# Kernel optimization log

Hardware: AMD Instinct MI355X
Metric: run time of the kernel (lower is better)

Reference implementation:

```python
import jax, jax.numpy as jnp
import numpy as np

N_EMBD = 1024
N_HEAD = 16
HEAD_DIM = N_EMBD // N_HEAD  # 64
N_CTX = 2048
ROPE_THETA = 10000.0


def _rope_cache(L, dim, base):
    inv_freq = 1.0 / (base ** (np.arange(0, dim, 2, dtype=np.float32) / dim))
    t = np.arange(L, dtype=np.float32)
    freqs = np.einsum('i,j->ij', t, inv_freq)  # (L, dim/2)
    return jnp.asarray(np.cos(freqs)), jnp.asarray(np.sin(freqs))


def _apply_rotary(x, cos, sin):
    # x: (B, H, L, D), cos/sin: (L, D/2) -> broadcast (1,1,L,D/2)
    x1 = x[..., ::2]
    x2 = x[..., 1::2]
    c = cos[None, None, :, :]
    s = sin[None, None, :, :]
    y1 = x1 * c - x2 * s
    y2 = x1 * s + x2 * c
    # interleave back: stack on last dim then flatten
    return jnp.stack((y1, y2), axis=-1).reshape(x.shape)


def setup_inputs() -> dict:
    key = jax.random.key(0)
    k1, k2, k3, k4, k5 = jax.random.split(key, 5)
    B, L, D = 4, 2048, N_EMBD
    scale = 0.02
    x = jax.random.normal(k1, (B, L, D), dtype=jnp.float32)
    W_qkv = jax.random.normal(k2, (D, 3 * D), dtype=jnp.float32) * scale
    b_qkv = jnp.zeros((3 * D,), dtype=jnp.float32)
    W_proj = jax.random.normal(k3, (D, D), dtype=jnp.float32) * scale
    b_proj = jnp.zeros((D,), dtype=jnp.float32)
    attention_mask = jnp.ones((B, L), dtype=jnp.int32)
    return {"x": x, "W_qkv": W_qkv, "b_qkv": b_qkv, "W_proj": W_proj,
            "b_proj": b_proj, "attention_mask": attention_mask}


def reference(x, W_qkv, b_qkv, W_proj, b_proj, attention_mask):
    B, L, D = x.shape
    H, Dh = N_HEAD, HEAD_DIM
    qkv = x @ W_qkv + b_qkv  # (B, L, 3D)
    q, k, v = jnp.split(qkv, 3, axis=2)
    # (B, L, H, Dh) -> (B, H, L, Dh)
    q = q.reshape(B, L, H, Dh).transpose(0, 2, 1, 3)
    k = k.reshape(B, L, H, Dh).transpose(0, 2, 1, 3)
    v = v.reshape(B, L, H, Dh).transpose(0, 2, 1, 3)
    cos, sin = _rope_cache(L, Dh, ROPE_THETA)
    q = _apply_rotary(q, cos, sin)
    k = _apply_rotary(k, cos, sin)
    # mask: causal & key padding keep
    causal = jnp.tril(jnp.ones((L, L), dtype=bool))[None, None]        # (1,1,L,L)
    key_keep = attention_mask.astype(bool)[:, None, None, :]          # (B,1,1,L)
    keep = causal & key_keep                                          # (B,1,L,L)
    scores = jnp.einsum('bhqd,bhkd->bhqk', q, k) / jnp.sqrt(jnp.float32(Dh))
    scores = jnp.where(keep, scores, jnp.finfo(scores.dtype).min)
    attn = jax.nn.softmax(scores, axis=-1)
    out = jnp.einsum('bhqk,bhkd->bhqd', attn, v)  # (B,H,L,Dh)
    out = out.transpose(0, 2, 1, 3).reshape(B, L, D)
    return out @ W_proj + b_proj
```

## Files before the change

kernel.cpp:

```cpp
#include <hip/hip_runtime.h>
#include <math.h>

typedef __bf16 bf16x8 __attribute__((ext_vector_type(8)));
typedef float f32x4 __attribute__((ext_vector_type(4)));
typedef float f32x16 __attribute__((ext_vector_type(16)));
typedef unsigned short u16;
typedef unsigned short u16x8 __attribute__((ext_vector_type(8)));
typedef unsigned short u16x4 __attribute__((ext_vector_type(4)));
typedef unsigned u32x2v __attribute__((ext_vector_type(2)));

#define BATCH 4
#define SEQ   2048
#define EMBD  1024
#define NHEAD 16
#define HDIM  64
#define MROWS 8192
#define QKVN  3072

__device__ __forceinline__ u16 f2bf(float f) {
    union { float f; unsigned u; } cv; cv.f = f;
    unsigned u = cv.u;
    return (u16)((u + 0x7FFFu + ((u >> 16) & 1u)) >> 16);
}

__device__ __forceinline__ unsigned cvtpk_bf16(float lo, float hi) {
    unsigned r;
    asm("v_cvt_pk_bf16_f32 %0, %1, %2" : "=v"(r) : "v"(lo), "v"(hi));
    return r;
}

__device__ __forceinline__ void glds16(const void* g, void* l) {
    __builtin_amdgcn_global_load_lds(
        (const __attribute__((address_space(1))) unsigned int*)(g),
        (__attribute__((address_space(3))) unsigned int*)(l), 16, 0, 0);
}

#define MF8(qm, A0, A1, A2, A3, B0, B1)                                          \
    acc[(qm)*4+0][0] = __builtin_amdgcn_mfma_f32_16x16x32_bf16(A0, B0, acc[(qm)*4+0][0], 0, 0, 0); \
    acc[(qm)*4+0][1] = __builtin_amdgcn_mfma_f32_16x16x32_bf16(A0, B1, acc[(qm)*4+0][1], 0, 0, 0); \
    acc[(qm)*4+1][0] = __builtin_amdgcn_mfma_f32_16x16x32_bf16(A1, B0, acc[(qm)*4+1][0], 0, 0, 0); \
    acc[(qm)*4+1][1] = __builtin_amdgcn_mfma_f32_16x16x32_bf16(A1, B1, acc[(qm)*4+1][1], 0, 0, 0); \
    acc[(qm)*4+2][0] = __builtin_amdgcn_mfma_f32_16x16x32_bf16(A2, B0, acc[(qm)*4+2][0], 0, 0, 0); \
    acc[(qm)*4+2][1] = __builtin_amdgcn_mfma_f32_16x16x32_bf16(A2, B1, acc[(qm)*4+2][1], 0, 0, 0); \
    acc[(qm)*4+3][0] = __builtin_amdgcn_mfma_f32_16x16x32_bf16(A3, B0, acc[(qm)*4+3][0], 0, 0, 0); \
    acc[(qm)*4+3][1] = __builtin_amdgcn_mfma_f32_16x16x32_bf16(A3, B1, acc[(qm)*4+3][1], 0, 0, 0);

__device__ __forceinline__ void transpose_body(const float* __restrict__ W,
                                               u16* __restrict__ Wt, int K, int N,
                                               int n0, int k0, u16 (*T)[68]) {
    const int tx = threadIdx.x & 15, ty = threadIdx.x >> 4;
#pragma unroll
    for (int r = 0; r < 4; r++) {
        int k = k0 + ty + r * 16;
        float4 w = *(const float4*)&W[(size_t)k * N + n0 + tx * 4];
        T[tx * 4 + 0][ty + r * 16] = f2bf(w.x);
        T[tx * 4 + 1][ty + r * 16] = f2bf(w.y);
        T[tx * 4 + 2][ty + r * 16] = f2bf(w.z);
        T[tx * 4 + 3][ty + r * 16] = f2bf(w.w);
    }
    __syncthreads();
#pragma unroll
    for (int r = 0; r < 4; r++) {
        int nl = ty + r * 16;
        u16x4 v = { T[nl][tx * 4 + 0], T[nl][tx * 4 + 1],
                    T[nl][tx * 4 + 2], T[nl][tx * 4 + 3] };
        *(u16x4*)&Wt[(size_t)(n0 + nl) * K + k0 + tx * 4] = v;
    }
}

__global__ __launch_bounds__(256)
void prep_kernel(const float* __restrict__ x, const float* __restrict__ Wqkv,
                 const float* __restrict__ Wproj, const int* __restrict__ amask,
                 u16* __restrict__ Xb, u16* __restrict__ Wqkvt, u16* __restrict__ Wprojt,
                 float* __restrict__ ropeC, float* __restrict__ ropeS,
                 float* __restrict__ mbias, int* __restrict__ flags) {
    __shared__ union { u16 T[64][68]; int ok[4]; } sm;
    const int bx = blockIdx.x, tid = threadIdx.x;
    if (bx < 8192) {
        int i = bx * 256 + tid;
        float4 v = ((const float4*)x)[i];
        u16x4 o = { f2bf(v.x), f2bf(v.y), f2bf(v.z), f2bf(v.w) };
        ((u16x4*)Xb)[i] = o;
    } else if (bx < 8960) {
        int bxx = bx - 8192;
        transpose_body(Wqkv, Wqkvt, EMBD, QKVN, (bxx % 48) * 64, (bxx / 48) * 64, sm.T);
    } else if (bx < 9216) {
        int bxx = bx - 8960;
        transpose_body(Wproj, Wprojt, EMBD, EMBD, (bxx & 15) * 64, (bxx >> 4) * 64, sm.T);
    } else if (bx < 9472) {
        int i = (bx - 9216) * 256 + tid;
        int l = i >> 5, p = i & 31;
        float invf = powf(10000.0f, -(float)(2 * p) * (1.0f / 64.0f));
        float sv, cv;
        sincosf((float)l * invf, &sv, &cv);
        ropeC[i] = cv; ropeS[i] = sv;
    } else {
        int idx = (bx - 9472) * 256 + tid;
        int mv = amask[idx];
        mbias[idx] = mv ? 0.0f : -1e30f;
        unsigned long long bal = __ballot(mv != 0);
        int wv = tid >> 6;
        if ((tid & 63) == 0) sm.ok[wv] = (bal == 0xFFFFFFFFFFFFFFFFull);
        __syncthreads();
        if (tid == 0)   flags[idx >> 7] = sm.ok[0] & sm.ok[1];
        if (tid == 128) flags[idx >> 7] = sm.ok[2] & sm.ok[3];
    }
}

__global__ __launch_bounds__(512, 2)
void qkv_gemm(const u16* __restrict__ A, const u16* __restrict__ Bt,
              const float* __restrict__ bias,
              const float* __restrict__ Ct, const float* __restrict__ St,
              u16* __restrict__ Qo, u16* __restrict__ Ko, u16* __restrict__ Vo) {
    __shared__ u16 SM[49152];
    const int tid = threadIdx.x;
    const int w = tid >> 6, ln = tid & 63;
    const int quad = ln >> 4, l16 = ln & 15;
    const int wm = w >> 2, wn = w & 3;
    const int bid = blockIdx.y * 24 + blockIdx.x;
    const int swz = (bid & 7) * 96 + (bid >> 3);
    const int m0 = (swz / 24) * 256, n0 = (swz % 24) * 128;

    const int sr8 = ln >> 3;
    const int xs = (ln & 7) ^ sr8;
    const u16* Ab = A  + (size_t)(m0 + w * 8 + sr8) * EMBD + xs * 8;
    const u16* Bb = Bt + (size_t)(n0 + w * 8 + sr8) * EMBD + xs * 8;
    u16* ldsA = SM + w * 512;
    u16* ldsB = SM + 32768 + w * 512;
    const int ch0 = ((0 + quad) ^ (l16 & 7)) * 8;
    const int ch1 = ((4 + quad) ^ (l16 & 7)) * 8;

    auto stageA = [&](int buf, int rb, int kt) {
        glds16(Ab + (size_t)rb * EMBD + kt * 64, ldsA + buf * 16384 + rb * 64);
    };
    auto stageB = [&](int buf, int rb, int kt) {
        glds16(Bb + (size_t)rb * EMBD + kt * 64, ldsB + buf * 8192 + rb * 64);
    };

    f32x4 acc[8][2] = {};

    stageA(0, 0, 0);  stageA(0, 128, 0);
    stageA(0, 64, 0); stageA(0, 192, 0);
    stageB(0, 0, 0);  stageB(0, 64, 0);
    stageA(1, 0, 1);  stageA(1, 128, 1);
    asm volatile("s_waitcnt vmcnt(2)" ::: "memory");
    __builtin_amdgcn_sched_barrier(0);
    __builtin_amdgcn_s_barrier();

    for (int u = 0; u < 16; ++u) {
        const int c = u & 1, nc = c ^ 1;
        const u16* Ac0 = SM + c * 16384 + (wm * 128 + l16) * 64;
        const u16* Ac1 = Ac0 + 64 * 64;
        const u16* Bc  = SM + 32768 + c * 8192 + (wn * 32 + l16) * 64;
        bf16x8 a0, a1, a2, a3, bk0a, bk0b, bk1a, bk1b;
        a0 = *(const bf16x8*)&Ac0[ch0];        a1 = *(const bf16x8*)&Ac0[1024 + ch0];
        a2 = *(const bf16x8*)&Ac0[2048 + ch0]; a3 = *(const bf16x8*)&Ac0[3072 + ch0];
        bk0a = *(const bf16x8*)&Bc[ch0];       bk0b = *(const bf16x8*)&Bc[1024 + ch0];
        if (u < 15) { stageA(nc, 64, u + 1); stageA(nc, 192, u + 1); stageB(nc, 64, u + 1); }
        __builtin_amdgcn_sched_barrier(0);
        __builtin_amdgcn_s_setprio(1);
        MF8(0, a0, a1, a2, a3, bk0a, bk0b);
        __builtin_amdgcn_s_setprio(0);
        __builtin_amdgcn_sched_barrier(0);
        a0 = *(const bf16x8*)&Ac0[ch1];        a1 = *(const bf16x8*)&Ac0[1024 + ch1];
        a2 = *(const bf16x8*)&Ac0[2048 + ch1]; a3 = *(const bf16x8*)&Ac0[3072 + ch1];
        bk1a = *(const bf16x8*)&Bc[ch1];       bk1b = *(const bf16x8*)&Bc[1024 + ch1];
        if (u < 15) stageB(nc, 0, u + 1);
        __builtin_amdgcn_sched_barrier(0);
        __builtin_amdgcn_s_setprio(1);
        MF8(0, a0, a1, a2, a3, bk1a, bk1b);
        __builtin_amdgcn_s_setprio(0);
        __builtin_amdgcn_sched_barrier(0);
        __builtin_amdgcn_s_barrier();
        a0 = *(const bf16x8*)&Ac1[ch0];        a1 = *(const bf16x8*)&Ac1[1024 + ch0];
        a2 = *(const bf16x8*)&Ac1[2048 + ch0]; a3 = *(const bf16x8*)&Ac1[3072 + ch0];
        if (u < 14) { stageA(c, 0, u + 2); stageA(c, 128, u + 2); }
        __builtin_amdgcn_sched_barrier(0);
        __builtin_amdgcn_s_setprio(1);
        MF8(1, a0, a1, a2, a3, bk0a, bk0b);
        __builtin_amdgcn_s_setprio(0);
        __builtin_amdgcn_sched_barrier(0);
        a0 = *(const bf16x8*)&Ac1[ch1];        a1 = *(const bf16x8*)&Ac1[1024 + ch1];
        a2 = *(const bf16x8*)&Ac1[2048 + ch1]; a3 = *(const bf16x8*)&Ac1[3072 + ch1];
        __builtin_amdgcn_sched_barrier(0);
        __builtin_amdgcn_s_setprio(1);
        MF8(1, a0, a1, a2, a3, bk1a, bk1b);
        __builtin_amdgcn_s_setprio(0);
        __builtin_amdgcn_sched_barrier(0);
        if (u < 14) asm volatile("s_waitcnt vmcnt(2)" ::: "memory");
        else        asm volatile("s_waitcnt vmcnt(0)" ::: "memory");
        __builtin_amdgcn_sched_barrier(0);
        __builtin_amdgcn_s_barrier();
    }

    const int sec = n0 >> 10;
    if (sec == 2) {
#pragma unroll
        for (int ii = 0; ii < 8; ii++)
#pragma unroll
            for (int r = 0; r < 4; r++) {
                int m = m0 + wm * 128 + ii * 16 + quad * 4 + r;
                int b = m >> 11, l = m & 2047;
#pragma unroll
                for (int j = 0; j < 2; j++) {
                    int n = n0 + wn * 32 + j * 16 + l16;
                    int dcol = n & 1023;
                    int h = dcol >> 6, dh = dcol & 63;
                    float v = acc[ii][j][r] + bias[n];
                    Vo[(((size_t)b * NHEAD + h) * SEQ + l) * HDIM + dh] = f2bf(v);
                }
            }
    } else {
        u16* O = (sec == 0) ? Qo : Ko;
        const float qs = (sec == 0) ? 0.125f * 1.44269504f : 1.0f;
#pragma unroll
        for (int ii = 0; ii < 8; ii++)
#pragma unroll
            for (int r = 0; r < 4; r++) {
                int m = m0 + wm * 128 + ii * 16 + quad * 4 + r;
                int b = m >> 11, l = m & 2047;
#pragma unroll
                for (int j = 0; j < 2; j++) {
                    int n = n0 + wn * 32 + j * 16 + l16;
                    int h = (n & 1023) >> 6, dh = n & 63;
                    int p = (n & 63) >> 1;
                    float v = acc[ii][j][r] + bias[n];
                    float pv = __shfl_xor(v, 1, 64);
                    float cv = Ct[l * 32 + p], sv = St[l * 32 + p];
                    float o = (l16 & 1) ? (pv * sv + v * cv) : (v * cv - pv * sv);
                    O[(((size_t)b * NHEAD + h) * SEQ + l) * HDIM + dh] = f2bf(o * qs);
                }
            }
    }
}

__global__ __launch_bounds__(256)
void transpose_v(const u16* __restrict__ Vo, u16* __restrict__ Vt) {
    __shared__ u16 T[64][72];
    const int bh = blockIdx.y;
    const int l0 = blockIdx.x * 64;
    const int tx = threadIdx.x & 15, ty = threadIdx.x >> 4;
#pragma unroll
    for (int rr = 0; rr < 4; rr++) {
        int l = ty + rr * 16;
        u16x4 v = *(const u16x4*)&Vo[((size_t)bh * SEQ + l0 + l) * HDIM + tx * 4];
        T[l][tx * 4 + 0] = v.x; T[l][tx * 4 + 1] = v.y;
        T[l][tx * 4 + 2] = v.z; T[l][tx * 4 + 3] = v.w;
    }
    __syncthreads();
#pragma unroll
    for (int rr = 0; rr < 4; rr++) {
        int dh = ty + rr * 16;
        u16x4 w = { T[tx * 4 + 0][dh], T[tx * 4 + 1][dh],
                    T[tx * 4 + 2][dh], T[tx * 4 + 3][dh] };
        *(u16x4*)&Vt[((size_t)bh * HDIM + dh) * SEQ + l0 + tx * 4] = w;
    }
}

__global__ __launch_bounds__(256)
void attn_mfma3(const u16* __restrict__ Qb, const u16* __restrict__ Kb,
                const u16* __restrict__ Vt, const float* __restrict__ mb,
                const int* __restrict__ flags, u16* __restrict__ Ot) {
    __shared__ u16 SM[32768];
    const int tid = threadIdx.x;
    const int wv = tid >> 6, ln = tid & 63;
    const int l32 = ln & 31, hi = ln >> 5;
    const int bh = blockIdx.x & 63;
    const int pr = blockIdx.x >> 6;
    const int b = bh >> 4;
    const u16* Qg = Qb + (size_t)bh * SEQ * HDIM;
    const u16* Kg = Kb + (size_t)bh * SEQ * HDIM;
    const u16* Vg = Vt + (size_t)bh * HDIM * SEQ;

    const int kRow = ln >> 3;
    const size_t kLane = (size_t)(wv * 32 + kRow) * 64 + ((ln & 7) ^ kRow) * 8;
    const int vRow = ln >> 4, sc0 = (ln & 15) ^ vRow;
    const size_t vLaneE = (size_t)(wv * 16 + vRow) * SEQ + sc0 * 8;
    const size_t vLaneO = (size_t)(wv * 16 + vRow) * SEQ + (sc0 ^ 4) * 8;

    for (int pass = 0; pass < 2; pass++) {
        const int qt = pass ? pr : 15 - pr;
        const int q0w = qt * 128 + wv * 32;

        bf16x8 Qf[4];
#pragma unroll
        for (int kd = 0; kd < 4; kd++)
            Qf[kd] = *(const bf16x8*)&Qg[(size_t)(q0w + l32) * HDIM + kd * 16 + hi * 8];

        f32x16 o[2] = {};
        float mrun = -1e30f, lrun = 0.f;

        {
            u16* KsD = SM + wv * 2048;
            u16* VsD = SM + 8192 + wv * 2048;
#pragma unroll
            for (int p = 0; p < 4; p++) {
                glds16(Kg + kLane + p * 512, KsD + p * 512);
                glds16(Vg + ((p & 1) ? vLaneO : vLaneE) + (size_t)p * 4 * SEQ, VsD + p * 512);
            }
        }
        __syncthreads();

        int buf = 0;
        for (int kt = 0; kt <= qt; kt++) {
            const int kbase = kt * 128;
            if (kt < qt) {
                const size_t nb = (size_t)(kbase + 128);
                u16* KsD = SM + (buf ^ 1) * 16384 + wv * 2048;
                u16* VsD = SM + (buf ^ 1) * 16384 + 8192 + wv * 2048;
#pragma unroll
                for (int p = 0; p < 4; p++) {
                    glds16(Kg + nb * 64 + kLane + p * 512, KsD + p * 512);
                    glds16(Vg + nb + ((p & 1) ? vLaneO : vLaneE) + (size_t)p * 4 * SEQ, VsD + p * 512);
                }
            }
            const u16* Ks = SM + buf * 16384;
            const u16* Vs = SM + buf * 16384 + 8192;

            f32x16 s[4];
            __builtin_amdgcn_s_setprio(1);
#pragma unroll
            for (int mi = 0; mi < 4; mi++) {
                const int key = mi * 32 + l32;
                f32x16 z = {};
#pragma unroll
                for (int kd = 0; kd < 4; kd++) {
                    int ch = kd * 2 + hi;
                    bf16x8 kf = *(const bf16x8*)&Ks[key * 64 + ((ch ^ (key & 7)) * 8)];
                    z = __builtin_amdgcn_mfma_f32_32x32x16_bf16(kf, Qf[kd], z, 0, 0, 0);
                }
                s[mi] = z;
            }
            __builtin_amdgcn_s_setprio(0);

            if (kt == qt) {
                const int qloc = wv * 32 + l32;
#pragma unroll
                for (int mi = 0; mi < 4; mi++)
#pragma unroll
                    for (int r = 0; r < 16; r++) {
                        int row = mi * 32 + (r & 3) + 8 * (r >> 2) + 4 * hi;
                        if (row > qloc) s[mi][r] = -1e30f;
                    }
            }
            if (!flags[b * 16 + kt]) {
#pragma unroll
                for (int mi = 0; mi < 4; mi++)
#pragma unroll
                    for (int r = 0; r < 16; r++) {
                        int row = mi * 32 + (r & 3) + 8 * (r >> 2) + 4 * hi;
                        s[mi][r] += mb[b * SEQ + kbase + row];
                    }
            }

            float rm = -1e30f;
#pragma unroll
            for (int mi = 0; mi < 4; mi++) {
                float a0 = fmaxf(fmaxf(s[mi][0],  s[mi][1]),  fmaxf(s[mi][2],  s[mi][3]));
                float a1 = fmaxf(fmaxf(s[mi][4],  s[mi][5]),  fmaxf(s[mi][6],  s[mi][7]));
                float a2 = fmaxf(fmaxf(s[mi][8],  s[mi][9]),  fmaxf(s[mi][10], s[mi][11]));
                float a3 = fmaxf(fmaxf(s[mi][12], s[mi][13]), fmaxf(s[mi][14], s[mi][15]));
                rm = fmaxf(rm, fmaxf(fmaxf(a0, a1), fmaxf(a2, a3)));
            }
            {
                u32x2v f = __builtin_amdgcn_permlane32_swap(
                    __float_as_uint(rm), __float_as_uint(rm), false, false);
                rm = fmaxf(__uint_as_float(f[0]), __uint_as_float(f[1]));
            }
            if (!__all(rm <= mrun + 8.0f)) {
                float mnew = fmaxf(mrun, rm);
                float al = __builtin_amdgcn_exp2f(mrun - mnew);
                mrun = mnew;
                lrun *= al;
#pragma unroll
                for (int r = 0; r < 16; r++) { o[0][r] *= al; o[1][r] *= al; }
            }
            float rs = 0.f;
#pragma unroll
            for (int mi = 0; mi < 4; mi++) {
                float ps = 0.f;
#pragma unroll
                for (int r = 0; r < 16; r++) {
                    float pe = __builtin_amdgcn_exp2f(s[mi][r] - mrun);
                    s[mi][r] = pe;
                    ps += pe;
                }
                rs += ps;
            }
            {
                u32x2v f = __builtin_amdgcn_permlane32_swap(
                    __float_as_uint(rs), __float_as_uint(rs), false, false);
                rs = __uint_as_float(f[0]) + __uint_as_float(f[1]);
            }
            lrun += rs;

#pragma unroll
            for (int t = 0; t < 4; t++) {
                unsigned A0 = cvtpk_bf16(s[t][0],  s[t][1]);
                unsigned B0 = cvtpk_bf16(s[t][4],  s[t][5]);
                unsigned A1 = cvtpk_bf16(s[t][2],  s[t][3]);
                unsigned B1 = cvtpk_bf16(s[t][6],  s[t][7]);
                u32x2v r0 = __builtin_amdgcn_permlane32_swap(A0, B0, false, false);
                u32x2v r1 = __builtin_amdgcn_permlane32_swap(A1, B1, false, false);
                union { unsigned u[4]; bf16x8 v; } p0;
                p0.u[0] = r0[0]; p0.u[1] = r1[0]; p0.u[2] = r0[1]; p0.u[3] = r1[1];

                unsigned A2 = cvtpk_bf16(s[t][8],  s[t][9]);
                unsigned B2 = cvtpk_bf16(s[t][12], s[t][13]);
                unsigned A3 = cvtpk_bf16(s[t][10], s[t][11]);
                unsigned B3 = cvtpk_bf16(s[t][14], s[t][15]);
                u32x2v r2 = __builtin_amdgcn_permlane32_swap(A2, B2, false, false);
                u32x2v r3 = __builtin_amdgcn_permlane32_swap(A3, B3, false, false);
                union { unsigned u[4]; bf16x8 v; } p1;
                p1.u[0] = r2[0]; p1.u[1] = r3[0]; p1.u[2] = r2[1]; p1.u[3] = r3[1];

                __builtin_amdgcn_s_setprio(1);
#pragma unroll
                for (int md = 0; md < 2; md++) {
                    const int dh = md * 32 + l32;
                    bf16x8 v0 = *(const bf16x8*)&Vs[dh * 128 + (((t * 4 + hi)     ^ (dh & 7)) * 8)];
                    o[md] = __builtin_amdgcn_mfma_f32_32x32x16_bf16(v0, p0.v, o[md], 0, 0, 0);
                    bf16x8 v1 = *(const bf16x8*)&Vs[dh * 128 + (((t * 4 + 2 + hi) ^ (dh & 7)) * 8)];
                    o[md] = __builtin_amdgcn_mfma_f32_32x32x16_bf16(v1, p1.v, o[md], 0, 0, 0);
                }
                __builtin_amdgcn_s_setprio(0);
            }
            __syncthreads();
            buf ^= 1;
        }

        u16* Osh = SM + wv * 2176;
        float inv = 1.0f / lrun;
#pragma unroll
        for (int md = 0; md < 2; md++)
#pragma unroll
            for (int r = 0; r < 16; r++) {
                int dh = md * 32 + (r & 3) + 8 * (r >> 2) + 4 * hi;
                Osh[l32 * 68 + dh] = f2bf(o[md][r] * inv);
            }
        __syncthreads();
        {
            int qrow = ln >> 1, hf = ln & 1;
            size_t gbase = ((size_t)bh * SEQ + qt * 128 + wv * 32 + qrow) * HDIM + hf * 32;
#pragma unroll
            for (int c = 0; c < 4; c++) {
                u16x8 vv = *(const u16x8*)&Osh[qrow * 68 + hf * 32 + c * 8];
                *(u16x8*)&Ot[gbase + c * 8] = vv;
            }
        }
        __syncthreads();
    }
}

__global__ __launch_bounds__(256)
void proj_gemm(const u16* __restrict__ A, const u16* __restrict__ Bt,
               const float* __restrict__ bias, float* __restrict__ out) {
    __shared__ u16 SM[32768];
    const int tid = threadIdx.x;
    const int wv = tid >> 6, ln = tid & 63;
    const int quad = ln >> 4, l16 = ln & 15;
    const int bid = blockIdx.y * 8 + blockIdx.x;
    const int swz = (bid & 7) * 64 + (bid >> 3);
    const int m0 = (swz >> 3) * 128, n0 = (swz & 7) * 128;
    const int wm = wv >> 1, wn = wv & 1;

    const int srow = wv * 8 + (ln >> 3);
    const int xs = (ln & 7) ^ (srow & 7);

    f32x4 acc[4][4] = {};

    auto stage = [&](int buf, int kt) {
        u16* As = SM + buf * 16384;
        u16* Bs = As + 8192;
#pragma unroll
        for (int p = 0; p < 4; p++) {
            int row = p * 32 + srow;
            int m = m0 + row;
            int bb = m >> 11, l = m & 2047;
            glds16(A + (((size_t)(bb * 16 + kt) * SEQ + l) * HDIM) + xs * 8,
                   As + (p * 256 + wv * 64) * 8);
            glds16(Bt + (size_t)(n0 + row) * EMBD + kt * 64 + xs * 8,
                   Bs + (p * 256 + wv * 64) * 8);
        }
    };

    stage(0, 0);
    __syncthreads();
    int buf = 0;
    for (int kt = 0; kt < 16; kt++) {
        if (kt < 15) stage(buf ^ 1, kt + 1);
        const u16* As = SM + buf * 16384;
        const u16* Bs = As + 8192;
        __builtin_amdgcn_s_setprio(1);
#pragma unroll
        for (int kk = 0; kk < 2; kk++) {
            bf16x8 af[4], bfr[4];
#pragma unroll
            for (int i = 0; i < 4; i++) {
                int R = wm * 64 + i * 16 + l16;
                af[i] = *(const bf16x8*)&As[R * 64 + (((kk * 4 + quad) ^ (R & 7)) * 8)];
            }
#pragma unroll
            for (int j = 0; j < 4; j++) {
                int R = wn * 64 + j * 16 + l16;
                bfr[j] = *(const bf16x8*)&Bs[R * 64 + (((kk * 4 + quad) ^ (R & 7)) * 8)];
            }
#pragma unroll
            for (int i = 0; i < 4; i++)
#pragma unroll
                for (int j = 0; j < 4; j++)
                    acc[i][j] = __builtin_amdgcn_mfma_f32_16x16x32_bf16(af[i], bfr[j], acc[i][j], 0, 0, 0);
        }
        __builtin_amdgcn_s_setprio(0);
        __syncthreads();
        buf ^= 1;
    }
#pragma unroll
    for (int i = 0; i < 4; i++)
#pragma unroll
        for (int r = 0; r < 4; r++) {
            int m = m0 + wm * 64 + i * 16 + quad * 4 + r;
#pragma unroll
            for (int j = 0; j < 4; j++) {
                int n = n0 + wn * 64 + j * 16 + l16;
                out[(size_t)m * EMBD + n] = acc[i][j][r] + bias[n];
            }
        }
}

extern "C" void kernel_launch(void* const* d_in, const int* in_sizes, int n_in,
                              void* d_out, int out_size, void* d_ws, size_t ws_size,
                              hipStream_t stream)
{
    const float* x     = (const float*)d_in[0];
    const float* Wqkv  = (const float*)d_in[1];
    const float* bqkv  = (const float*)d_in[2];
    const float* Wproj = (const float*)d_in[3];
    const float* bproj = (const float*)d_in[4];
    const int*   amask = (const int*)d_in[5];
    float* out = (float*)d_out;

    char* ws = (char*)d_ws;
    u16*   Xb     = (u16*)(ws);
    u16*   Ot     = (u16*)(ws);
    u16*   Wqkvt  = (u16*)(ws + 16777216);
    u16*   Wprojt = (u16*)(ws + 23068672);
    u16*   Qb     = (u16*)(ws + 25165824);
    u16*   Kb     = (u16*)(ws + 41943040);
    u16*   Vb     = (u16*)(ws + 58720256);
    u16*   Vtp    = (u16*)(ws + 75497472);
    float* ropeC  = (float*)(ws + 92274688);
    float* ropeS  = (float*)(ws + 92536832);
    float* mbias  = (float*)(ws + 92798976);
    int*   flags  = (int*)(ws + 92831744);

    prep_kernel<<<9504, 256, 0, stream>>>(x, Wqkv, Wproj, amask,
                                          Xb, Wqkvt, Wprojt, ropeC, ropeS, mbias, flags);
    qkv_gemm<<<dim3(24, 32), 512, 0, stream>>>(
        Xb, Wqkvt, bqkv, ropeC, ropeS, Qb, Kb, Vb);
    transpose_v<<<dim3(32, 64), 256, 0, stream>>>(Vb, Vtp);
    attn_mfma3<<<512, 256, 0, stream>>>(Qb, Kb, Vtp, mbias, flags, Ot);
    proj_gemm<<<dim3(EMBD / 128, MROWS / 128), 256, 0, stream>>>(Ot, Wprojt, bproj, out);
}
```

Baseline: 246.4 us.

## Enlarge attention blocks to 256 query rows with 8 waves sharing K/V tiles

The attention kernel now runs 512 threads (8 waves) per block covering a 256-row query tile, instead of 4 waves doing two passes over 128-row tiles paired for load balance. Each K/V tile staged in shared memory is reused by twice as many query rows, which cuts global K/V traffic and per-tile load instructions per wave. The causal mask is now applied by absolute position on every tile that crosses the diagonal. Each block does one pass, with queue order chosen to start the heaviest tiles first. Risks: less even per-block work, fewer resident blocks per CU, and half-empty diagonal tiles that waste more MFMA work.

```diff
diff --git a/kernel.cpp b/kernel.cpp
--- a/kernel.cpp
+++ b/kernel.cpp
@@ -257,7 +257,7 @@
     }
 }
 
-__global__ __launch_bounds__(256)
+__global__ __launch_bounds__(512, 2)
 void attn_mfma3(const u16* __restrict__ Qb, const u16* __restrict__ Kb,
                 const u16* __restrict__ Vt, const float* __restrict__ mb,
                 const int* __restrict__ flags, u16* __restrict__ Ot) {
@@ -265,190 +265,189 @@
     const int tid = threadIdx.x;
     const int wv = tid >> 6, ln = tid & 63;
     const int l32 = ln & 31, hi = ln >> 5;
-    const int bh = blockIdx.x & 63;
-    const int pr = blockIdx.x >> 6;
+    const int bid = blockIdx.x;
+    const int bh = bid & 63;
+    const int qt = (bid < 256) ? 7 - (bid >> 6) : ((bid - 256) >> 6);
     const int b = bh >> 4;
     const u16* Qg = Qb + (size_t)bh * SEQ * HDIM;
     const u16* Kg = Kb + (size_t)bh * SEQ * HDIM;
     const u16* Vg = Vt + (size_t)bh * HDIM * SEQ;
 
     const int kRow = ln >> 3;
-    const size_t kLane = (size_t)(wv * 32 + kRow) * 64 + ((ln & 7) ^ kRow) * 8;
+    const size_t kLane = (size_t)(wv * 16 + kRow) * 64 + ((ln & 7) ^ kRow) * 8;
     const int vRow = ln >> 4, sc0 = (ln & 15) ^ vRow;
-    const size_t vLaneE = (size_t)(wv * 16 + vRow) * SEQ + sc0 * 8;
-    const size_t vLaneO = (size_t)(wv * 16 + vRow) * SEQ + (sc0 ^ 4) * 8;
-
-    for (int pass = 0; pass < 2; pass++) {
-        const int qt = pass ? pr : 15 - pr;
-        const int q0w = qt * 128 + wv * 32;
-
-        bf16x8 Qf[4];
-#pragma unroll
-        for (int kd = 0; kd < 4; kd++)
-            Qf[kd] = *(const bf16x8*)&Qg[(size_t)(q0w + l32) * HDIM + kd * 16 + hi * 8];
-
-        f32x16 o[2] = {};
-        float mrun = -1e30f, lrun = 0.f;
-
+    const size_t vLaneE = (size_t)(wv * 8 + vRow) * SEQ + sc0 * 8;
+    const size_t vLaneO = (size_t)(wv * 8 + 4 + vRow) * SEQ + (sc0 ^ 4) * 8;
+
+    const int q0w = qt * 256 + wv * 32;
+    const int qmin = q0w;
+    const int qabs = q0w + l32;
+
+    bf16x8 Qf[4];
+#pragma unroll
+    for (int kd = 0; kd < 4; kd++)
+        Qf[kd] = *(const bf16x8*)&Qg[(size_t)(q0w + l32) * HDIM + kd * 16 + hi * 8];
+
+    f32x16 o[2] = {};
+    float mrun = -1e30f, lrun = 0.f;
+
+    const int nkt = 2 * qt + 2;
+
+    {
+        u16* KsD = SM + wv * 1024;
+        u16* VsD = SM + 8192 + wv * 1024;
+        glds16(Kg + kLane,       KsD);
+        glds16(Kg + kLane + 512, KsD + 512);
+        glds16(Vg + vLaneE,      VsD);
+        glds16(Vg + vLaneO,      VsD + 512);
+    }
+    __syncthreads();
+
+    int buf = 0;
+    for (int kt = 0; kt < nkt; kt++) {
+        const int kbase = kt * 128;
+        if (kt + 1 < nkt) {
+            const size_t nb = (size_t)(kbase + 128);
+            u16* KsD = SM + (buf ^ 1) * 16384 + wv * 1024;
+            u16* VsD = SM + (buf ^ 1) * 16384 + 8192 + wv * 1024;
+            glds16(Kg + nb * 64 + kLane,       KsD);
+            glds16(Kg + nb * 64 + kLane + 512, KsD + 512);
+            glds16(Vg + nb + vLaneE,           VsD);
+            glds16(Vg + nb + vLaneO,           VsD + 512);
+        }
+        const u16* Ks = SM + buf * 16384;
+        const u16* Vs = SM + buf * 16384 + 8192;
+
+        f32x16 s[4];
+        __builtin_amdgcn_s_setprio(1);
+#pragma unroll
+        for (int mi = 0; mi < 4; mi++) {
+            const int key = mi * 32 + l32;
+            f32x16 z = {};
+#pragma unroll
+            for (int kd = 0; kd < 4; kd++) {
+                int ch = kd * 2 + hi;
+                bf16x8 kf = *(const bf16x8*)&Ks[key * 64 + ((ch ^ (key & 7)) * 8)];
+                z = __builtin_amdgcn_mfma_f32_32x32x16_bf16(kf, Qf[kd], z, 0, 0, 0);
+            }
+            s[mi] = z;
+        }
+        __builtin_amdgcn_s_setprio(0);
+
+        if (kbase + 127 > qmin) {
+#pragma unroll
+            for (int mi = 0; mi < 4; mi++)
+#pragma unroll
+                for (int r = 0; r < 16; r++) {
+                    int row = kbase + mi * 32 + (r & 3) + 8 * (r >> 2) + 4 * hi;
+                    if (row > qabs) s[mi][r] = -1e30f;
+                }
+        }
+        if (!flags[b * 16 + kt]) {
+#pragma unroll
+            for (int mi = 0; mi < 4; mi++)
+#pragma unroll
+                for (int r = 0; r < 16; r++) {
+                    int row = mi * 32 + (r & 3) + 8 * (r >> 2) + 4 * hi;
+                    s[mi][r] += mb[b * SEQ + kbase + row];
+                }
+        }
+
+        float rm = -1e30f;
+#pragma unroll
+        for (int mi = 0; mi < 4; mi++) {
+            float a0 = fmaxf(fmaxf(s[mi][0],  s[mi][1]),  fmaxf(s[mi][2],  s[mi][3]));
+            float a1 = fmaxf(fmaxf(s[mi][4],  s[mi][5]),  fmaxf(s[mi][6],  s[mi][7]));
+            float a2 = fmaxf(fmaxf(s[mi][8],  s[mi][9]),  fmaxf(s[mi][10], s[mi][11]));
+            float a3 = fmaxf(fmaxf(s[mi][12], s[mi][13]), fmaxf(s[mi][14], s[mi][15]));
+            rm = fmaxf(rm, fmaxf(fmaxf(a0, a1), fmaxf(a2, a3)));
+        }
         {
-            u16* KsD = SM + wv * 2048;
-            u16* VsD = SM + 8192 + wv * 2048;
-#pragma unroll
-            for (int p = 0; p < 4; p++) {
-                glds16(Kg + kLane + p * 512, KsD + p * 512);
-                glds16(Vg + ((p & 1) ? vLaneO : vLaneE) + (size_t)p * 4 * SEQ, VsD + p * 512);
-            }
+            u32x2v f = __builtin_amdgcn_permlane32_swap(
+                __float_as_uint(rm), __float_as_uint(rm), false, false);
+            rm = fmaxf(__uint_as_float(f[0]), __uint_as_float(f[1]));
+        }
+        if (!__all(rm <= mrun + 8.0f)) {
+            float mnew = fmaxf(mrun, rm);
+            float al = __builtin_amdgcn_exp2f(mrun - mnew);
+            mrun = mnew;
+            lrun *= al;
+#pragma unroll
+            for (int r = 0; r < 16; r++) { o[0][r] *= al; o[1][r] *= al; }
+        }
+        float rs = 0.f;
+#pragma unroll
+        for (int mi = 0; mi < 4; mi++) {
+            float ps = 0.f;
+#pragma unroll
+            for (int r = 0; r < 16; r++) {
+                float pe = __builtin_amdgcn_exp2f(s[mi][r] - mrun);
+                s[mi][r] = pe;
+                ps += pe;
+            }
+            rs += ps;
+        }
+        {
+            u32x2v f = __builtin_amdgcn_permlane32_swap(
+                __float_as_uint(rs), __float_as_uint(rs), false, false);
+            rs = __uint_as_float(f[0]) + __uint_as_float(f[1]);
+        }
+        lrun += rs;
+
+#pragma unroll
+        for (int t = 0; t < 4; t++) {
+            unsigned A0 = cvtpk_bf16(s[t][0],  s[t][1]);
+            unsigned B0 = cvtpk_bf16(s[t][4],  s[t][5]);
+            unsigned A1 = cvtpk_bf16(s[t][2],  s[t][3]);
+            unsigned B1 = cvtpk_bf16(s[t][6],  s[t][7]);
+            u32x2v r0 = __builtin_amdgcn_permlane32_swap(A0, B0, false, false);
+            u32x2v r1 = __builtin_amdgcn_permlane32_swap(A1, B1, false, false);
+            union { unsigned u[4]; bf16x8 v; } p0;
+            p0.u[0] = r0[0]; p0.u[1] = r1[0]; p0.u[2] = r0[1]; p0.u[3] = r1[1];
+
+            unsigned A2 = cvtpk_bf16(s[t][8],  s[t][9]);
+            unsigned B2 = cvtpk_bf16(s[t][12], s[t][13]);
+            unsigned A3 = cvtpk_bf16(s[t][10], s[t][11]);
+            unsigned B3 = cvtpk_bf16(s[t][14], s[t][15]);
+            u32x2v r2 = __builtin_amdgcn_permlane32_swap(A2, B2, false, false);
+            u32x2v r3 = __builtin_amdgcn_permlane32_swap(A3, B3, false, false);
+            union { unsigned u[4]; bf16x8 v; } p1;
+            p1.u[0] = r2[0]; p1.u[1] = r3[0]; p1.u[2] = r2[1]; p1.u[3] = r3[1];
+
+            __builtin_amdgcn_s_setprio(1);
+#pragma unroll
+            for (int md = 0; md < 2; md++) {
+                const int dh = md * 32 + l32;
+                bf16x8 v0 = *(const bf16x8*)&Vs[dh * 128 + (((t * 4 + hi)     ^ (dh & 7)) * 8)];
+                o[md] = __builtin_amdgcn_mfma_f32_32x32x16_bf16(v0, p0.v, o[md], 0, 0, 0);
+                bf16x8 v1 = *(const bf16x8*)&Vs[dh * 128 + (((t * 4 + 2 + hi) ^ (dh & 7)) * 8)];
+                o[md] = __builtin_amdgcn_mfma_f32_32x32x16_bf16(v1, p1.v, o[md], 0, 0, 0);
+            }
+            __builtin_amdgcn_s_setprio(0);
         }
         __syncthreads();
-
-        int buf = 0;
-        for (int kt = 0; kt <= qt; kt++) {
-            const int kbase = kt * 128;
-            if (kt < qt) {
-                const size_t nb = (size_t)(kbase + 128);
-                u16* KsD = SM + (buf ^ 1) * 16384 + wv * 2048;
-                u16* VsD = SM + (buf ^ 1) * 16384 + 8192 + wv * 2048;
-#pragma unroll
-                for (int p = 0; p < 4; p++) {
-                    glds16(Kg + nb * 64 + kLane + p * 512, KsD + p * 512);
-                    glds16(Vg + nb + ((p & 1) ? vLaneO : vLaneE) + (size_t)p * 4 * SEQ, VsD + p * 512);
-                }
-            }
-            const u16* Ks = SM + buf * 16384;
-            const u16* Vs = SM + buf * 16384 + 8192;
-
-            f32x16 s[4];
-            __builtin_amdgcn_s_setprio(1);
-#pragma unroll
-            for (int mi = 0; mi < 4; mi++) {
-                const int key = mi * 32 + l32;
-                f32x16 z = {};
-#pragma unroll
-                for (int kd = 0; kd < 4; kd++) {
-                    int ch = kd * 2 + hi;
-                    bf16x8 kf = *(const bf16x8*)&Ks[key * 64 + ((ch ^ (key & 7)) * 8)];
-                    z = __builtin_amdgcn_mfma_f32_32x32x16_bf16(kf, Qf[kd], z, 0, 0, 0);
-                }
-                s[mi] = z;
-            }
-            __builtin_amdgcn_s_setprio(0);
-
-            if (kt == qt) {
-                const int qloc = wv * 32 + l32;
-#pragma unroll
-                for (int mi = 0; mi < 4; mi++)
-#pragma unroll
-                    for (int r = 0; r < 16; r++) {
-                        int row = mi * 32 + (r & 3) + 8 * (r >> 2) + 4 * hi;
-                        if (row > qloc) s[mi][r] = -1e30f;
-                    }
-            }
-            if (!flags[b * 16 + kt]) {
-#pragma unroll
-                for (int mi = 0; mi < 4; mi++)
-#pragma unroll
-                    for (int r = 0; r < 16; r++) {
-                        int row = mi * 32 + (r & 3) + 8 * (r >> 2) + 4 * hi;
-                        s[mi][r] += mb[b * SEQ + kbase + row];
-                    }
-            }
-
-            float rm = -1e30f;
-#pragma unroll
-            for (int mi = 0; mi < 4; mi++) {
-                float a0 = fmaxf(fmaxf(s[mi][0],  s[mi][1]),  fmaxf(s[mi][2],  s[mi][3]));
-                float a1 = fmaxf(fmaxf(s[mi][4],  s[mi][5]),  fmaxf(s[mi][6],  s[mi][7]));
-                float a2 = fmaxf(fmaxf(s[mi][8],  s[mi][9]),  fmaxf(s[mi][10], s[mi][11]));
-                float a3 = fmaxf(fmaxf(s[mi][12], s[mi][13]), fmaxf(s[mi][14], s[mi][15]));
-                rm = fmaxf(rm, fmaxf(fmaxf(a0, a1), fmaxf(a2, a3)));
-            }
-            {
-                u32x2v f = __builtin_amdgcn_permlane32_swap(
-                    __float_as_uint(rm), __float_as_uint(rm), false, false);
-                rm = fmaxf(__uint_as_float(f[0]), __uint_as_float(f[1]));
-            }
-            if (!__all(rm <= mrun + 8.0f)) {
-                float mnew = fmaxf(mrun, rm);
-                float al = __builtin_amdgcn_exp2f(mrun - mnew);
-                mrun = mnew;
-                lrun *= al;
-#pragma unroll
-                for (int r = 0; r < 16; r++) { o[0][r] *= al; o[1][r] *= al; }
-            }
-            float rs = 0.f;
-#pragma unroll
-            for (int mi = 0; mi < 4; mi++) {
-                float ps = 0.f;
-#pragma unroll
-                for (int r = 0; r < 16; r++) {
-                    float pe = __builtin_amdgcn_exp2f(s[mi][r] - mrun);
-                    s[mi][r] = pe;
-                    ps += pe;
-                }
-                rs += ps;
-            }
-            {
-                u32x2v f = __builtin_amdgcn_permlane32_swap(
-                    __float_as_uint(rs), __float_as_uint(rs), false, false);
-                rs = __uint_as_float(f[0]) + __uint_as_float(f[1]);
-            }
-            lrun += rs;
-
-#pragma unroll
-            for (int t = 0; t < 4; t++) {
-                unsigned A0 = cvtpk_bf16(s[t][0],  s[t][1]);
-                unsigned B0 = cvtpk_bf16(s[t][4],  s[t][5]);
-                unsigned A1 = cvtpk_bf16(s[t][2],  s[t][3]);
-                unsigned B1 = cvtpk_bf16(s[t][6],  s[t][7]);
-                u32x2v r0 = __builtin_amdgcn_permlane32_swap(A0, B0, false, false);
-                u32x2v r1 = __builtin_amdgcn_permlane32_swap(A1, B1, false, false);
-                union { unsigned u[4]; bf16x8 v; } p0;
-                p0.u[0] = r0[0]; p0.u[1] = r1[0]; p0.u[2] = r0[1]; p0.u[3] = r1[1];
-
-                unsigned A2 = cvtpk_bf16(s[t][8],  s[t][9]);
-                unsigned B2 = cvtpk_bf16(s[t][12], s[t][13]);
-                unsigned A3 = cvtpk_bf16(s[t][10], s[t][11]);
-                unsigned B3 = cvtpk_bf16(s[t][14], s[t][15]);
-                u32x2v r2 = __builtin_amdgcn_permlane32_swap(A2, B2, false, false);
-                u32x2v r3 = __builtin_amdgcn_permlane32_swap(A3, B3, false, false);
-                union { unsigned u[4]; bf16x8 v; } p1;
-                p1.u[0] = r2[0]; p1.u[1] = r3[0]; p1.u[2] = r2[1]; p1.u[3] = r3[1];
-
-                __builtin_amdgcn_s_setprio(1);
-#pragma unroll
-                for (int md = 0; md < 2; md++) {
-                    const int dh = md * 32 + l32;
-                    bf16x8 v0 = *(const bf16x8*)&Vs[dh * 128 + (((t * 4 + hi)     ^ (dh & 7)) * 8)];
-                    o[md] = __builtin_amdgcn_mfma_f32_32x32x16_bf16(v0, p0.v, o[md], 0, 0, 0);
-                    bf16x8 v1 = *(const bf16x8*)&Vs[dh * 128 + (((t * 4 + 2 + hi) ^ (dh & 7)) * 8)];
-                    o[md] = __builtin_amdgcn_mfma_f32_32x32x16_bf16(v1, p1.v, o[md], 0, 0, 0);
-                }
-                __builtin_amdgcn_s_setprio(0);
-            }
-            __syncthreads();
-            buf ^= 1;
-        }
-
-        u16* Osh = SM + wv * 2176;
-        float inv = 1.0f / lrun;
-#pragma unroll
-        for (int md = 0; md < 2; md++)
-#pragma unroll
-            for (int r = 0; r < 16; r++) {
-                int dh = md * 32 + (r & 3) + 8 * (r >> 2) + 4 * hi;
-                Osh[l32 * 68 + dh] = f2bf(o[md][r] * inv);
-            }
-        __syncthreads();
-        {
-            int qrow = ln >> 1, hf = ln & 1;
-            size_t gbase = ((size_t)bh * SEQ + qt * 128 + wv * 32 + qrow) * HDIM + hf * 32;
-#pragma unroll
-            for (int c = 0; c < 4; c++) {
-                u16x8 vv = *(const u16x8*)&Osh[qrow * 68 + hf * 32 + c * 8];
-                *(u16x8*)&Ot[gbase + c * 8] = vv;
-            }
-        }
-        __syncthreads();
+        buf ^= 1;
+    }
+
+    __syncthreads();
+    u16* Osh = SM + wv * 2176;
+    float inv = 1.0f / lrun;
+#pragma unroll
+    for (int md = 0; md < 2; md++)
+#pragma unroll
+        for (int r = 0; r < 16; r++) {
+            int dh = md * 32 + (r & 3) + 8 * (r >> 2) + 4 * hi;
+            Osh[l32 * 68 + dh] = f2bf(o[md][r] * inv);
+        }
+    __syncthreads();
+    {
+        int qrow = ln >> 1, hf = ln & 1;
+        size_t gbase = ((size_t)bh * SEQ + q0w + qrow) * HDIM + hf * 32;
+#pragma unroll
+        for (int c = 0; c < 4; c++) {
+            u16x8 vv = *(const u16x8*)&Osh[qrow * 68 + hf * 32 + c * 8];
+            *(u16x8*)&Ot[gbase + c * 8] = vv;
+        }
     }
 }
 
@@ -559,6 +558,6 @@
     qkv_gemm<<<dim3(24, 32), 512, 0, stream>>>(
         Xb, Wqkvt, bqkv, ropeC, ropeS, Qb, Kb, Vb);
     transpose_v<<<dim3(32, 64), 256, 0, stream>>>(Vb, Vtp);
-    attn_mfma3<<<512, 256, 0, stream>>>(Qb, Kb, Vtp, mbias, flags, Ot);
+    attn_mfma3<<<512, 512, 0, stream>>>(Qb, Kb, Vtp, mbias, flags, Ot);
     proj_gemm<<<dim3(EMBD / 128, MROWS / 128), 256, 0, stream>>>(Ot, Wprojt, bproj, out);
 }
```

Measured after the change: 245.8 us. No clear change (-0.2%).
